# Kernel optimization log

Measured on AMD Instinct MI355X. Metric: run time of the kernel, lower is better.

Reference implementation:

```python
import jax, jax.numpy as jnp
import numpy as np

N_PREV = 250_000   # rows of `features` / `coors` (voxels at previous scale)
N_FULL = 500_000   # full raw points (coors_inv_full / scale_coors_inv length)
V = 65_536         # voxels at current scale
C_IN = 64
C_OUT = 64
SCALE = 2
EPS = 1e-5


def lrelu(x):
    return jnp.where(x > 0, x, 0.1 * x)


def masked_bn(x, mask, gamma, beta):
    # training-mode BatchNorm1d over valid (non-padded) rows only; mask: [M,1]
    n = jnp.maximum(mask.sum(), 1.0)
    mu = (x * mask).sum(0) / n
    var = (((x - mu) * mask) ** 2).sum(0) / n  # biased var, as torch BN
    return gamma * (x - mu) * jax.lax.rsqrt(var + EPS) + beta


def setup_inputs():
    key = jax.random.key(0)
    ks = jax.random.split(key, 16)
    features = jax.random.normal(ks[0], (N_PREV, C_IN), jnp.float32)
    batch = jax.random.randint(ks[1], (N_PREV, 1), 0, 4)
    xy = jax.random.randint(ks[2], (N_PREV, 2), 0, 1000)
    z = jax.random.randint(ks[3], (N_PREV, 1), 0, 60)
    coors = jnp.concatenate([batch, xy, z], axis=1).astype(jnp.int32)
    coors_inv_full = jax.random.randint(ks[4], (N_FULL,), 0, N_PREV, jnp.int32)
    scale_coors_inv = jax.random.randint(ks[5], (N_FULL,), 0, V, jnp.int32)

    def lin(k, i, o):
        return jax.random.normal(k, (i, o), jnp.float32) / np.sqrt(i).astype(np.float32)

    h = C_OUT // 2
    return dict(
        features=features, coors=coors, coors_inv_full=coors_inv_full,
        scale_coors_inv=scale_coors_inv,
        W_in=lin(ks[6], C_IN, C_OUT), b_in=jnp.zeros((C_OUT,), jnp.float32),
        W1=lin(ks[7], C_IN, h), b1=jnp.zeros((h,), jnp.float32),
        g1=jnp.ones((h,), jnp.float32), be1=jnp.zeros((h,), jnp.float32),
        W2=lin(ks[8], h, h), b2=jnp.zeros((h,), jnp.float32),
        g2=jnp.ones((h,), jnp.float32), be2=jnp.zeros((h,), jnp.float32),
        W3=lin(ks[9], h, C_OUT), b3=jnp.zeros((C_OUT,), jnp.float32),
        Wo1=lin(ks[10], 2 * C_OUT, C_OUT), bo1=jnp.zeros((C_OUT,), jnp.float32),
        Wo2=lin(ks[11], C_OUT, C_OUT), bo2=jnp.zeros((C_OUT,), jnp.float32),
    )


def reference(features, coors, coors_inv_full, scale_coors_inv,
              W_in, b_in, W1, b1, g1, be1, W2, b2, g2, be2, W3, b3,
              Wo1, bo1, Wo2, bo2):
    # --- downsample: unique voxel key + scatter_mean (torch.unique return_inverse) ---
    b = coors[:, 0].astype(jnp.int32)
    xyz = coors[:, 1:].astype(jnp.int32) // SCALE
    keys = ((b * 501 + xyz[:, 0]) * 501 + xyz[:, 1]) * 31 + xyz[:, 2]  # < 2^31
    _, inv = jnp.unique(keys, return_inverse=True, size=N_PREV,
                        fill_value=jnp.int32(2**31 - 1))
    cnt = jax.ops.segment_sum(jnp.ones((N_PREV,), jnp.float32), inv,
                              num_segments=N_PREV)
    pooled = jax.ops.segment_sum(features, inv, num_segments=N_PREV) \
        / jnp.maximum(cnt, 1.0)[:, None]
    valid = (cnt > 0).astype(jnp.float32)[:, None]

    # --- identity branch: layer_in ---
    identity = lrelu(features @ W_in + b_in)

    # --- PPmodel on pooled voxels, then gather back by inv ---
    h = masked_bn(lrelu(pooled @ W1 + b1), valid, g1, be1)
    h = masked_bn(lrelu(h @ W2 + b2), valid, g2, be2)
    h = lrelu(h @ W3 + b3)
    out = jnp.concatenate([identity, h[inv]], axis=1)  # [N_PREV, 2*C_OUT]

    # --- gather to full points, layer_out, scatter_mean to scale voxels ---
    gathered = out[coors_inv_full]                      # [N_FULL, 2*C_OUT]
    po = lrelu(gathered @ Wo1 + bo1) @ Wo2 + bo2        # [N_FULL, C_OUT]
    cnt_v = jax.ops.segment_sum(jnp.ones((N_FULL,), jnp.float32),
                                scale_coors_inv, num_segments=V)
    v_feat = jax.ops.segment_sum(po, scale_coors_inv, num_segments=V) \
        / jnp.maximum(cnt_v, 1.0)[:, None]
    return v_feat
```

## Files before the change

### kernel.cpp

```cpp
#include <hip/hip_runtime.h>

#define N_PREV 250000
#define N_FULL 500000
#define NVOX   65536
#define NWORDS (1u<<20)
#define EPSF   1e-5f

typedef __attribute__((ext_vector_type(4)))  short short4v;
typedef __attribute__((ext_vector_type(8)))  short short8v;
typedef __attribute__((ext_vector_type(16))) float f32x16;

__device__ __forceinline__ float lrelu(float x){ return x > 0.0f ? x : 0.1f*x; }
__device__ __forceinline__ short f2bf_rne(float v){
    unsigned u = __float_as_uint(v);
    unsigned r = (u + 0x7fffu + ((u>>16)&1u)) >> 16;
    return (short)r;
}
__device__ __forceinline__ float bf2f(short s){
    return __uint_as_float(((unsigned)(unsigned short)s) << 16);
}

#define OFF_BITMAP   0ul
#define OFF_STATS    4194304ul
#define OFF_CNT      4195328ul
#define OFF_VH       5195328ul
#define OFF_Y        5457472ul
#define ZERO_BYTES   21457472ul
#define OFF_T        5457472ul
#define OFF_P2       37457472ul
#define OFF_PREF     69457472ul
#define OFF_BSUM     73651776ul
#define OFF_BOFF     73655872ul
#define OFF_UCNT     73659968ul
#define OFF_INV      73660224ul
#define OFF_P1       74660224ul
#define OFF_X2       106660224ul
#define WS_NEEDED    138660224ul
#define OFF_CSRJ     0ul
#define OFF_CSRH     2000000ul
#define OFF_VSTART   69457472ul
#define OFF_VNEXT    (OFF_VSTART+262400ul)
#define OFF_VPART    (OFF_VNEXT+262144ul)
#define OFF_VBSUM    (OFF_VPART+262144ul)

__device__ __forceinline__ int voxel_key(int4 c){
    return ((c.x*501 + (c.y>>1))*501 + (c.z>>1))*31 + (c.w>>1);
}

__global__ void k_mark(const int* __restrict__ coors, unsigned* __restrict__ bitmap){
    int i = blockIdx.x*256 + threadIdx.x;
    if(i >= N_PREV) return;
    int4 c = ((const int4*)coors)[i];
    int key = voxel_key(c);
    atomicOr(&bitmap[key>>5], 1u<<(key&31));
}

__global__ void __launch_bounds__(1024) k_scanA(const unsigned* __restrict__ bitmap,
                                                unsigned* __restrict__ pref,
                                                unsigned* __restrict__ bsum){
    __shared__ unsigned sh[1024];
    int tid = threadIdx.x;
    int w = blockIdx.x*1024 + tid;
    unsigned p = __popc(bitmap[w]);
    sh[tid] = p; __syncthreads();
    for(int off=1; off<1024; off<<=1){
        unsigned v = (tid>=off) ? sh[tid-off] : 0u;
        __syncthreads();
        sh[tid] += v;
        __syncthreads();
    }
    pref[w] = sh[tid] - p;
    if(tid==1023) bsum[blockIdx.x] = sh[tid];
}

__global__ void __launch_bounds__(1024) k_scanB(const unsigned* __restrict__ bsum,
                                                unsigned* __restrict__ boff,
                                                unsigned* __restrict__ Ucnt){
    __shared__ unsigned sh[1024];
    int tid = threadIdx.x;
    unsigned p = bsum[tid];
    sh[tid] = p; __syncthreads();
    for(int off=1; off<1024; off<<=1){
        unsigned v = (tid>=off) ? sh[tid-off] : 0u;
        __syncthreads();
        sh[tid] += v;
        __syncthreads();
    }
    boff[tid] = sh[tid] - p;
    if(tid==1023) Ucnt[0] = sh[tid];
}

__global__ void k_vhist(const int* __restrict__ scv, unsigned* __restrict__ vh){
    int p = blockIdx.x*256 + threadIdx.x;
    if(p < N_FULL) atomicAdd(&vh[scv[p]], 1u);
}

__global__ void __launch_bounds__(1024) k_vscanA(const unsigned* __restrict__ vh,
                                                 unsigned* __restrict__ vpart,
                                                 unsigned* __restrict__ vbsum){
    __shared__ unsigned sh[1024];
    int tid = threadIdx.x;
    int w = blockIdx.x*1024 + tid;
    unsigned p = vh[w];
    sh[tid] = p; __syncthreads();
    for(int off=1; off<1024; off<<=1){
        unsigned v = (tid>=off) ? sh[tid-off] : 0u;
        __syncthreads();
        sh[tid] += v;
        __syncthreads();
    }
    vpart[w] = sh[tid] - p;
    if(tid==1023) vbsum[blockIdx.x] = sh[tid];
}

__global__ void k_vscanB(unsigned* __restrict__ vbsum){
    int l = threadIdx.x;
    unsigned v = vbsum[l], orig = v;
    for(int off=1; off<64; off<<=1){
        unsigned o = __shfl_up(v, off);
        if(l>=off) v += o;
    }
    vbsum[l] = v - orig;
}

__global__ void __launch_bounds__(1024) k_vfix(const unsigned* __restrict__ vpart,
                                               const unsigned* __restrict__ vbsum,
                                               unsigned* __restrict__ vstart,
                                               unsigned* __restrict__ vnext){
    int w = blockIdx.x*1024 + threadIdx.x;
    unsigned s = vpart[w] + vbsum[w>>10];
    vstart[w] = s; vnext[w] = s;
    if(w == NVOX-1) vstart[NVOX] = N_FULL;
}

__global__ void k_fill(const int* __restrict__ cif, const int* __restrict__ scv,
                       const int* __restrict__ inv, unsigned* __restrict__ vnext,
                       int* __restrict__ csr_j, int* __restrict__ csr_h){
    int p = blockIdx.x*256 + threadIdx.x;
    if(p >= N_FULL) return;
    int jp = cif[p];
    unsigned pos = atomicAdd(&vnext[scv[p]], 1u);
    csr_j[pos] = jp;
    csr_h[pos] = inv[jp];
}

__global__ void __launch_bounds__(256) k_p1f(const float* __restrict__ feat,
        const int* __restrict__ coors, const unsigned* __restrict__ bitmap,
        const unsigned* __restrict__ pref, const unsigned* __restrict__ boff,
        const float* __restrict__ Win, const float* __restrict__ bin,
        const float* __restrict__ Wo1, const float* __restrict__ W1,
        unsigned short* __restrict__ P1, int* __restrict__ inv,
        float* __restrict__ cnt, unsigned short* __restrict__ yb){
    __shared__ __align__(16) short Ah[64*68];
    __shared__ __align__(16) short Al[64*68];
    __shared__ float ysh[64][33];
    __shared__ int rksh[64];
    int tid = threadIdx.x;
    int wave = tid >> 6, l = tid & 63;
    int g = l >> 5, c = l & 31;
    int rowhalf = (wave >> 1) * 32, colhalf = (wave & 1) * 32;

    {
        int col = tid >> 2, kseg = (tid & 3) * 16;
        short hi[16], lo[16];
        #pragma unroll
        for(int j=0;j<16;++j){
            float v = Win[(kseg+j)*64 + col];
            short h = f2bf_rne(v);
            hi[j] = h; lo[j] = f2bf_rne(v - bf2f(h));
        }
        #pragma unroll
        for(int i=0;i<4;++i){
            *(short4v*)&Ah[col*68 + kseg + 4*i] = *(short4v*)&hi[4*i];
            *(short4v*)&Al[col*68 + kseg + 4*i] = *(short4v*)&lo[4*i];
        }
    }
    __syncthreads();
    short8v w1h[4], w1l[4];
    #pragma unroll
    for(int s=0;s<4;++s){
        int base = (colhalf + c)*68 + s*16 + g*4;
        ((short4v*)&w1h[s])[0] = *(short4v*)&Ah[base];
        ((short4v*)&w1h[s])[1] = *(short4v*)&Ah[base + 8];
        ((short4v*)&w1l[s])[0] = *(short4v*)&Al[base];
        ((short4v*)&w1l[s])[1] = *(short4v*)&Al[base + 8];
    }
    __syncthreads();
    {
        int col = tid >> 2, kseg = (tid & 3) * 16;
        short hi[16];
        #pragma unroll
        for(int j=0;j<16;++j) hi[j] = f2bf_rne(Wo1[(kseg+j)*64 + col]);
        #pragma unroll
        for(int i=0;i<4;++i)
            *(short4v*)&Ah[col*68 + kseg + 4*i] = *(short4v*)&hi[4*i];
    }
    __syncthreads();
    short8v w2h[4];
    #pragma unroll
    for(int s=0;s<4;++s){
        int base = (colhalf + c)*68 + s*16 + g*4;
        ((short4v*)&w2h[s])[0] = *(short4v*)&Ah[base];
        ((short4v*)&w2h[s])[1] = *(short4v*)&Ah[base + 8];
    }
    __syncthreads();
    if(tid < 128){
        int col = tid >> 2, kseg = (tid & 3) * 16;
        short hi[16], lo[16];
        #pragma unroll
        for(int j=0;j<16;++j){
            float v = W1[(kseg+j)*32 + col];
            short h = f2bf_rne(v);
            hi[j] = h; lo[j] = f2bf_rne(v - bf2f(h));
        }
        #pragma unroll
        for(int i=0;i<4;++i){
            *(short4v*)&Ah[col*68 + kseg + 4*i] = *(short4v*)&hi[4*i];
            *(short4v*)&Al[col*68 + kseg + 4*i] = *(short4v*)&lo[4*i];
        }
    }
    __syncthreads();
    short8v w0h[4], w0l[4];
    #pragma unroll
    for(int s=0;s<4;++s){
        int base = c*68 + s*16 + g*4;
        ((short4v*)&w0h[s])[0] = *(short4v*)&Ah[base];
        ((short4v*)&w0h[s])[1] = *(short4v*)&Ah[base + 8];
        ((short4v*)&w0l[s])[0] = *(short4v*)&Al[base];
        ((short4v*)&w0l[s])[1] = *(short4v*)&Al[base + 8];
    }
    __syncthreads();

    float bc1 = bin[colhalf + c];

    const int NT = (N_PREV + 63) / 64;
    for(int tile = blockIdx.x; tile < NT; tile += gridDim.x){
        int rbase = tile * 64;
        {
            int row = tid >> 2, kseg = (tid & 3) * 16;
            int grow = rbase + row;
            float fv[16];
            if(grow < N_PREV){
                const float4* fp = (const float4*)&feat[grow*64 + kseg];
                *(float4*)&fv[0]  = fp[0];
                *(float4*)&fv[4]  = fp[1];
                *(float4*)&fv[8]  = fp[2];
                *(float4*)&fv[12] = fp[3];
            } else {
                #pragma unroll
                for(int j=0;j<16;++j) fv[j]=0.f;
            }
            short hi[16], lo[16];
            #pragma unroll
            for(int j=0;j<16;++j){
                short h = f2bf_rne(fv[j]);
                hi[j] = h; lo[j] = f2bf_rne(fv[j] - bf2f(h));
            }
            #pragma unroll
            for(int i=0;i<4;++i){
                *(short4v*)&Ah[row*68 + kseg + 4*i] = *(short4v*)&hi[4*i];
                *(short4v*)&Al[row*68 + kseg + 4*i] = *(short4v*)&lo[4*i];
            }
        }
        if(tid < 64){
            int grow = rbase + tid;
            if(grow < N_PREV){
                int4 c4 = ((const int4*)coors)[grow];
                int key = voxel_key(c4);
                int w = key>>5, b = key&31;
                int rank = (int)(boff[w>>10] + pref[w]) + __popc(bitmap[w] & ((1u<<b)-1u));
                rksh[tid] = rank;
                inv[grow] = rank;
                atomicAdd(&cnt[rank], 1.0f);
            } else rksh[tid] = -1;
        }
        __syncthreads();
        f32x16 acc;
        #pragma unroll
        for(int i=0;i<16;++i) acc[i]=0.f;
        #pragma unroll
        for(int s=0;s<4;++s){
            int abase = (rowhalf + c)*68 + s*16 + g*4;
            short8v ah, al;
            ((short4v*)&ah)[0] = *(short4v*)&Ah[abase];
            ((short4v*)&ah)[1] = *(short4v*)&Ah[abase + 8];
            ((short4v*)&al)[0] = *(short4v*)&Al[abase];
            ((short4v*)&al)[1] = *(short4v*)&Al[abase + 8];
            acc = __builtin_amdgcn_mfma_f32_32x32x16_bf16(ah, w1h[s], acc, 0,0,0);
            acc = __builtin_amdgcn_mfma_f32_32x32x16_bf16(al, w1h[s], acc, 0,0,0);
            acc = __builtin_amdgcn_mfma_f32_32x32x16_bf16(ah, w1l[s], acc, 0,0,0);
        }
        f32x16 accY;
        #pragma unroll
        for(int i=0;i<16;++i) accY[i]=0.f;
        if(wave < 2){
            #pragma unroll
            for(int s=0;s<4;++s){
                int abase = (wave*32 + c)*68 + s*16 + g*4;
                short8v ah, al;
                ((short4v*)&ah)[0] = *(short4v*)&Ah[abase];
                ((short4v*)&ah)[1] = *(short4v*)&Ah[abase + 8];
                ((short4v*)&al)[0] = *(short4v*)&Al[abase];
                ((short4v*)&al)[1] = *(short4v*)&Al[abase + 8];
                accY = __builtin_amdgcn_mfma_f32_32x32x16_bf16(ah, w0h[s], accY, 0,0,0);
                accY = __builtin_amdgcn_mfma_f32_32x32x16_bf16(al, w0h[s], accY, 0,0,0);
                accY = __builtin_amdgcn_mfma_f32_32x32x16_bf16(ah, w0l[s], accY, 0,0,0);
            }
        }
        __syncthreads();
        #pragma unroll
        for(int r=0;r<16;++r){
            int row = rowhalf + (r&3) + 8*(r>>2) + 4*g;
            float v = acc[r] + bc1;
            v = v > 0.f ? v : 0.1f*v;
            Ah[row*68 + colhalf + c] = f2bf_rne(v);
        }
        if(wave < 2){
            #pragma unroll
            for(int r=0;r<16;++r){
                int row = wave*32 + (r&3) + 8*(r>>2) + 4*g;
                ysh[row][c] = accY[r];
            }
        }
        __syncthreads();
        f32x16 acc2;
        #pragma unroll
        for(int i=0;i<16;++i) acc2[i]=0.f;
        #pragma unroll
        for(int s=0;s<4;++s){
            int abase = (rowhalf + c)*68 + s*16 + g*4;
            short8v ah;
            ((short4v*)&ah)[0] = *(short4v*)&Ah[abase];
            ((short4v*)&ah)[1] = *(short4v*)&Ah[abase + 8];
            acc2 = __builtin_amdgcn_mfma_f32_32x32x16_bf16(ah, w2h[s], acc2, 0,0,0);
        }
        #pragma unroll
        for(int r=0;r<16;++r){
            int grow = rbase + rowhalf + (r&3) + 8*(r>>2) + 4*g;
            if(grow < N_PREV) P1[grow*64 + colhalf + c] = (unsigned short)f2bf_rne(acc2[r]);
        }
        #pragma unroll
        for(int q=0;q<4;++q){
            int e = q*256 + tid;
            int row = e >> 4, pr = e & 15;
            int rk = rksh[row];
            if(rk >= 0){
                unsigned h0 = (unsigned)(unsigned short)f2bf_rne(ysh[row][2*pr]);
                unsigned h1 = (unsigned)(unsigned short)f2bf_rne(ysh[row][2*pr+1]);
                unsigned pk = h0 | (h1 << 16);
                unsigned short* addr = yb + (size_t)rk*32 + 2*pr;
                asm volatile("global_atomic_pk_add_bf16 %0, %1, off"
                             :: "v"(addr), "v"(pk) : "memory");
            }
        }
        __syncthreads();
    }
}

__global__ void __launch_bounds__(256) k_bn1(const unsigned short* __restrict__ yb,
        const float* __restrict__ cnt, const unsigned* __restrict__ Ucnt,
        const float* __restrict__ b1, float* __restrict__ stats){
    __shared__ float sst[32], qst[32];
    int tid = threadIdx.x;
    if(tid < 32){ sst[tid]=0.f; qst[tid]=0.f; }
    __syncthreads();
    int U = (int)Ucnt[0];
    int total = U*4;
    int c8 = (tid&3)*8;
    float bb[8];
    #pragma unroll
    for(int j=0;j<8;++j) bb[j] = b1[c8+j];
    float s[8], q[8];
    #pragma unroll
    for(int j=0;j<8;++j){ s[j]=0.f; q[j]=0.f; }
    for(int e = blockIdx.x*256 + tid; e < total; e += gridDim.x*256){
        int row = e >> 2;
        float rv = 1.0f/cnt[row];
        uint4 a = ((const uint4*)yb)[e];
        unsigned wv[4] = {a.x,a.y,a.z,a.w};
        #pragma unroll
        for(int k=0;k<4;++k){
            float lo = __uint_as_float(wv[k]<<16);
            float hi = __uint_as_float(wv[k]&0xffff0000u);
            float v0 = lrelu(lo*rv + bb[2*k]);
            float v1 = lrelu(hi*rv + bb[2*k+1]);
            s[2*k]+=v0; q[2*k]+=v0*v0;
            s[2*k+1]+=v1; q[2*k+1]+=v1*v1;
        }
    }
    #pragma unroll
    for(int j=0;j<8;++j){ atomicAdd(&sst[c8+j], s[j]); atomicAdd(&qst[c8+j], q[j]); }
    __syncthreads();
    if(tid < 32){ atomicAdd(&stats[tid], sst[tid]); atomicAdd(&stats[32+tid], qst[tid]); }
}

__global__ void k_bnfin(const unsigned* __restrict__ Ucnt, const float* __restrict__ g,
                        float* __restrict__ stats, int off){
    int c = threadIdx.x;
    if(c>=32) return;
    float n = (float)max(Ucnt[0], 1u);
    float mu = stats[off+c]/n;
    float var = stats[off+32+c]/n - mu*mu;
    stats[off+64+c] = mu;
    stats[off+96+c] = g[c]*rsqrtf(var + EPSF);
}

__global__ void __launch_bounds__(256) k_ppm2(const unsigned short* __restrict__ yb,
        const float* __restrict__ cnt, const unsigned* __restrict__ Ucnt,
        const float* __restrict__ W2, const float* __restrict__ b1i,
        const float* __restrict__ b2, const float* __restrict__ be1,
        unsigned short* __restrict__ x2b, float* __restrict__ stats){
    __shared__ __align__(16) short Ah[128*36];
    __shared__ __align__(16) short Al[128*36];
    __shared__ float ash[32], bbsh[32], b1sh[32];
    __shared__ float red[4][64];
    int tid = threadIdx.x;
    int wave = tid >> 6, l = tid & 63;
    int g = l >> 5, c = l & 31;

    if(tid < 32){
        float mu=stats[64+tid], sc=stats[96+tid];
        ash[tid]=sc; bbsh[tid]=be1[tid]-mu*sc;
        b1sh[tid]=b1i[tid];
    }
    if(tid >= 64 && tid < 128){
        int t = tid - 64;
        int col = t >> 1, kseg = (t & 1) * 16;
        short hi[16], lo[16];
        #pragma unroll
        for(int j=0;j<16;++j){
            float v = W2[(kseg+j)*32 + col];
            short h = f2bf_rne(v);
            hi[j] = h; lo[j] = f2bf_rne(v - bf2f(h));
        }
        #pragma unroll
        for(int i=0;i<4;++i){
            *(short4v*)&Ah[col*36 + kseg + 4*i] = *(short4v*)&hi[4*i];
            *(short4v*)&Al[col*36 + kseg + 4*i] = *(short4v*)&lo[4*i];
        }
    }
    __syncthreads();
    short8v wh[2], wl[2];
    #pragma unroll
    for(int s=0;s<2;++s){
        int base = c*36 + s*16 + g*4;
        ((short4v*)&wh[s])[0] = *(short4v*)&Ah[base];
        ((short4v*)&wh[s])[1] = *(short4v*)&Ah[base + 8];
        ((short4v*)&wl[s])[0] = *(short4v*)&Al[base];
        ((short4v*)&wl[s])[1] = *(short4v*)&Al[base + 8];
    }
    __syncthreads();

    int U = (int)Ucnt[0];
    float bc = b2[c];
    float s_acc = 0.f, q_acc = 0.f;

    const int NT = (N_PREV + 127) / 128;
    for(int tile = blockIdx.x; tile < NT; tile += gridDim.x){
        int rbase = tile * 128;
        if(rbase >= U) break;
        {
            int row = tid >> 1, kseg = (tid & 1) * 16;
            int grow = rbase + row;
            float fv[16];
            if(grow < U){
                float rv = 1.0f/cnt[grow];
                uint4 a0 = *(const uint4*)&yb[grow*32 + kseg];
                uint4 a1 = *(const uint4*)&yb[grow*32 + kseg + 8];
                unsigned wv[8] = {a0.x,a0.y,a0.z,a0.w,a1.x,a1.y,a1.z,a1.w};
                #pragma unroll
                for(int k=0;k<8;++k){
                    float lo = __uint_as_float(wv[k]<<16);
                    float hi = __uint_as_float(wv[k]&0xffff0000u);
                    float v0 = lrelu(lo*rv + b1sh[kseg+2*k]);
                    float v1 = lrelu(hi*rv + b1sh[kseg+2*k+1]);
                    fv[2*k]   = v0*ash[kseg+2*k]   + bbsh[kseg+2*k];
                    fv[2*k+1] = v1*ash[kseg+2*k+1] + bbsh[kseg+2*k+1];
                }
            } else {
                #pragma unroll
                for(int j=0;j<16;++j) fv[j]=0.f;
            }
            short hi[16], lo[16];
            #pragma unroll
            for(int j=0;j<16;++j){
                short h = f2bf_rne(fv[j]);
                hi[j] = h; lo[j] = f2bf_rne(fv[j] - bf2f(h));
            }
            #pragma unroll
            for(int i=0;i<4;++i){
                *(short4v*)&Ah[row*36 + kseg + 4*i] = *(short4v*)&hi[4*i];
                *(short4v*)&Al[row*36 + kseg + 4*i] = *(short4v*)&lo[4*i];
            }
        }
        __syncthreads();
        f32x16 acc;
        #pragma unroll
        for(int i=0;i<16;++i) acc[i]=0.f;
        #pragma unroll
        for(int s=0;s<2;++s){
            int abase = (wave*32 + c)*36 + s*16 + g*4;
            short8v ah, al;
            ((short4v*)&ah)[0] = *(short4v*)&Ah[abase];
            ((short4v*)&ah)[1] = *(short4v*)&Ah[abase + 8];
            ((short4v*)&al)[0] = *(short4v*)&Al[abase];
            ((short4v*)&al)[1] = *(short4v*)&Al[abase + 8];
            acc = __builtin_amdgcn_mfma_f32_32x32x16_bf16(ah, wh[s], acc, 0,0,0);
            acc = __builtin_amdgcn_mfma_f32_32x32x16_bf16(al, wh[s], acc, 0,0,0);
            acc = __builtin_amdgcn_mfma_f32_32x32x16_bf16(ah, wl[s], acc, 0,0,0);
        }
        #pragma unroll
        for(int r=0;r<16;++r){
            int rl = wave*32 + (r&3) + 8*(r>>2) + 4*g;
            int grow = rbase + rl;
            if(grow < U){
                float v = acc[r] + bc;
                v = v > 0.f ? v : 0.1f*v;
                x2b[grow*32 + c] = (unsigned short)f2bf_rne(v);
                s_acc += v; q_acc += v*v;
            }
        }
        __syncthreads();
    }
    s_acc += __shfl_xor(s_acc, 32);
    q_acc += __shfl_xor(q_acc, 32);
    if(l < 32){ red[wave][c] = s_acc; red[wave][32+c] = q_acc; }
    __syncthreads();
    if(tid < 64){
        float t = red[0][tid]+red[1][tid]+red[2][tid]+red[3][tid];
        atomicAdd(&stats[128+tid], t);
    }
}

__global__ void __launch_bounds__(256) k_ppm3(const unsigned short* __restrict__ x2b,
        const unsigned* __restrict__ Ucnt, const float* __restrict__ W3,
        const float* __restrict__ b3, const float* __restrict__ be2,
        const float* __restrict__ Wo1, unsigned short* __restrict__ P2,
        const float* __restrict__ stats){
    __shared__ __align__(16) short Ah[64*36];
    __shared__ __align__(16) short Al[64*36];
    __shared__ __align__(16) short Ih[64*68];
    __shared__ __align__(16) short Il[64*36];
    __shared__ float ash[32], bbsh[32];
    int tid = threadIdx.x;
    int wave = tid >> 6, l = tid & 63;
    int g = l >> 5, c = l & 31;
    int rowhalf = (wave >> 1) * 32, colhalf = (wave & 1) * 32;

    if(tid < 32){
        float mu=stats[192+tid], sc=stats[224+tid];
        ash[tid]=sc; bbsh[tid]=be2[tid]-mu*sc;
    }
    if(tid >= 128){
        int t = tid - 128;
        int col = t >> 1, kseg = (t & 1) * 16;
        short hi[16], lo[16];
        #pragma unroll
        for(int j=0;j<16;++j){
            float v = W3[(kseg+j)*64 + col];
            short h = f2bf_rne(v);
            hi[j] = h; lo[j] = f2bf_rne(v - bf2f(h));
        }
        #pragma unroll
        for(int i=0;i<4;++i){
            *(short4v*)&Ih[col*36 + kseg + 4*i] = *(short4v*)&hi[4*i];
            *(short4v*)&Il[col*36 + kseg + 4*i] = *(short4v*)&lo[4*i];
        }
    }
    __syncthreads();
    short8v w3h[2], w3l[2];
    #pragma unroll
    for(int s=0;s<2;++s){
        int base = (colhalf + c)*36 + s*16 + g*4;
        ((short4v*)&w3h[s])[0] = *(short4v*)&Ih[base];
        ((short4v*)&w3h[s])[1] = *(short4v*)&Ih[base + 8];
        ((short4v*)&w3l[s])[0] = *(short4v*)&Il[base];
        ((short4v*)&w3l[s])[1] = *(short4v*)&Il[base + 8];
    }
    __syncthreads();
    {
        int col = tid >> 2, kseg = (tid & 3) * 16;
        short hi[16];
        #pragma unroll
        for(int j=0;j<16;++j) hi[j] = f2bf_rne(Wo1[4096 + (kseg+j)*64 + col]);
        #pragma unroll
        for(int i=0;i<4;++i)
            *(short4v*)&Ih[col*68 + kseg + 4*i] = *(short4v*)&hi[4*i];
    }
    __syncthreads();
    short8v w2h[4];
    #pragma unroll
    for(int s=0;s<4;++s){
        int base = (colhalf + c)*68 + s*16 + g*4;
        ((short4v*)&w2h[s])[0] = *(short4v*)&Ih[base];
        ((short4v*)&w2h[s])[1] = *(short4v*)&Ih[base + 8];
    }
    __syncthreads();

    int U = (int)Ucnt[0];
    float bc3 = b3[colhalf + c];

    const int NT = (N_PREV + 63) / 64;
    for(int tile = blockIdx.x; tile < NT; tile += gridDim.x){
        int rbase = tile * 64;
        if(rbase >= U) break;
        if(tid < 128){
            int row = tid >> 1, kseg = (tid & 1) * 16;
            int grow = rbase + row;
            float fv[16];
            if(grow < U){
                uint4 a0 = *(const uint4*)&x2b[grow*32 + kseg];
                uint4 a1 = *(const uint4*)&x2b[grow*32 + kseg + 8];
                unsigned wv[8] = {a0.x,a0.y,a0.z,a0.w,a1.x,a1.y,a1.z,a1.w};
                #pragma unroll
                for(int k=0;k<8;++k){
                    float lo = __uint_as_float(wv[k]<<16);
                    float hi = __uint_as_float(wv[k]&0xffff0000u);
                    fv[2*k]   = lo*ash[kseg+2*k]   + bbsh[kseg+2*k];
                    fv[2*k+1] = hi*ash[kseg+2*k+1] + bbsh[kseg+2*k+1];
                }
            } else {
                #pragma unroll
                for(int j=0;j<16;++j) fv[j]=0.f;
            }
            short hi[16], lo[16];
            #pragma unroll
            for(int j=0;j<16;++j){
                short h = f2bf_rne(fv[j]);
                hi[j] = h; lo[j] = f2bf_rne(fv[j] - bf2f(h));
            }
            #pragma unroll
            for(int i=0;i<4;++i){
                *(short4v*)&Ah[row*36 + kseg + 4*i] = *(short4v*)&hi[4*i];
                *(short4v*)&Al[row*36 + kseg + 4*i] = *(short4v*)&lo[4*i];
            }
        }
        __syncthreads();
        f32x16 acc;
        #pragma unroll
        for(int i=0;i<16;++i) acc[i]=0.f;
        #pragma unroll
        for(int s=0;s<2;++s){
            int abase = (rowhalf + c)*36 + s*16 + g*4;
            short8v ah, al;
            ((short4v*)&ah)[0] = *(short4v*)&Ah[abase];
            ((short4v*)&ah)[1] = *(short4v*)&Ah[abase + 8];
            ((short4v*)&al)[0] = *(short4v*)&Al[abase];
            ((short4v*)&al)[1] = *(short4v*)&Al[abase + 8];
            acc = __builtin_amdgcn_mfma_f32_32x32x16_bf16(ah, w3h[s], acc, 0,0,0);
            acc = __builtin_amdgcn_mfma_f32_32x32x16_bf16(al, w3h[s], acc, 0,0,0);
            acc = __builtin_amdgcn_mfma_f32_32x32x16_bf16(ah, w3l[s], acc, 0,0,0);
        }
        #pragma unroll
        for(int r=0;r<16;++r){
            int row = rowhalf + (r&3) + 8*(r>>2) + 4*g;
            float v = acc[r] + bc3;
            v = v > 0.f ? v : 0.1f*v;
            Ih[row*68 + colhalf + c] = f2bf_rne(v);
        }
        __syncthreads();
        f32x16 acc2;
        #pragma unroll
        for(int i=0;i<16;++i) acc2[i]=0.f;
        #pragma unroll
        for(int s=0;s<4;++s){
            int abase = (rowhalf + c)*68 + s*16 + g*4;
            short8v ah;
            ((short4v*)&ah)[0] = *(short4v*)&Ih[abase];
            ((short4v*)&ah)[1] = *(short4v*)&Ih[abase + 8];
            acc2 = __builtin_amdgcn_mfma_f32_32x32x16_bf16(ah, w2h[s], acc2, 0,0,0);
        }
        #pragma unroll
        for(int r=0;r<16;++r){
            int grow = rbase + rowhalf + (r&3) + 8*(r>>2) + 4*g;
            if(grow < U) P2[grow*64 + colhalf + c] = (unsigned short)f2bf_rne(acc2[r]);
        }
        __syncthreads();
    }
}

__global__ void __launch_bounds__(256) k_vox(const unsigned* __restrict__ vstart,
        const int* __restrict__ csr_j, const int* __restrict__ csr_h,
        const unsigned short* __restrict__ P1, const unsigned short* __restrict__ P2,
        const float* __restrict__ bo1, float* __restrict__ T){
    int tid = threadIdx.x;
    int wib = tid>>6, lane = tid&63;
    float b1c = bo1[lane];
    int wglobal = blockIdx.x*4 + wib;
    for(int vq=0; vq<4; ++vq){
        int vox = wglobal*4 + vq;
        int s = (int)vstart[vox], e = (int)vstart[vox+1];
        float acc = 0.f;
        for(int i=s; i<e; i+=64){
            int n = min(e-i, 64);
            int jv=0, hv=0;
            if(lane<n){ jv = csr_j[i+lane]; hv = csr_h[i+lane]; }
            for(int q0=0; q0<n; q0+=8){
                float pa[8], pb[8];
                #pragma unroll
                for(int t=0;t<8;++t){
                    int qq = q0 + t;
                    qq = (qq < n) ? qq : q0;
                    int j = __shfl(jv, qq);
                    int h = __shfl(hv, qq);
                    pa[t] = bf2f((short)P1[(size_t)j*64 + lane]);
                    pb[t] = bf2f((short)P2[(size_t)h*64 + lane]);
                }
                #pragma unroll
                for(int t=0;t<8;++t){
                    if(q0 + t < n){
                        float g = pa[t] + pb[t] + b1c;
                        acc += (g>0.f) ? g : 0.1f*g;
                    }
                }
            }
        }
        T[(size_t)vox*64 + lane] = acc;
    }
}

__global__ void __launch_bounds__(256) k_wo2(const float* __restrict__ T,
        const unsigned* __restrict__ vstart, const float* __restrict__ Wo2,
        const float* __restrict__ bo2, float* __restrict__ out){
    __shared__ __align__(16) short Ah[64*68];
    __shared__ __align__(16) short Al[64*68];
    __shared__ float csh[64];
    int tid = threadIdx.x;
    int wave = tid >> 6, l = tid & 63;
    int g = l >> 5, c = l & 31;
    int rowhalf = (wave >> 1) * 32, colhalf = (wave & 1) * 32;

    {
        int col = tid >> 2, kseg = (tid & 3) * 16;
        short hi[16], lo[16];
        #pragma unroll
        for(int j=0;j<16;++j){
            float v = Wo2[(kseg+j)*64 + col];
            short h = f2bf_rne(v);
            hi[j] = h; lo[j] = f2bf_rne(v - bf2f(h));
        }
        #pragma unroll
        for(int i=0;i<4;++i){
            *(short4v*)&Ah[col*68 + kseg + 4*i] = *(short4v*)&hi[4*i];
            *(short4v*)&Al[col*68 + kseg + 4*i] = *(short4v*)&lo[4*i];
        }
    }
    __syncthreads();
    short8v wh[4], wl[4];
    #pragma unroll
    for(int s=0;s<4;++s){
        int base = (colhalf + c)*68 + s*16 + g*4;
        ((short4v*)&wh[s])[0] = *(short4v*)&Ah[base];
        ((short4v*)&wh[s])[1] = *(short4v*)&Ah[base + 8];
        ((short4v*)&wl[s])[0] = *(short4v*)&Al[base];
        ((short4v*)&wl[s])[1] = *(short4v*)&Al[base + 8];
    }
    __syncthreads();

    float bo2c = bo2[colhalf + c];

    const int NT = NVOX / 64;
    for(int tile = blockIdx.x; tile < NT; tile += gridDim.x){
        int rbase = tile * 64;
        {
            int row = tid >> 2, kseg = (tid & 3) * 16;
            const float4* fp = (const float4*)&T[(size_t)(rbase + row)*64 + kseg];
            float fv[16];
            *(float4*)&fv[0]  = fp[0];
            *(float4*)&fv[4]  = fp[1];
            *(float4*)&fv[8]  = fp[2];
            *(float4*)&fv[12] = fp[3];
            short hi[16], lo[16];
            #pragma unroll
            for(int j=0;j<16;++j){
                short h = f2bf_rne(fv[j]);
                hi[j] = h; lo[j] = f2bf_rne(fv[j] - bf2f(h));
            }
            #pragma unroll
            for(int i=0;i<4;++i){
                *(short4v*)&Ah[row*68 + kseg + 4*i] = *(short4v*)&hi[4*i];
                *(short4v*)&Al[row*68 + kseg + 4*i] = *(short4v*)&lo[4*i];
            }
        }
        if(tid < 64){
            int vox = rbase + tid;
            csh[tid] = (float)(vstart[vox+1] - vstart[vox]);
        }
        __syncthreads();
        f32x16 acc;
        #pragma unroll
        for(int i=0;i<16;++i) acc[i]=0.f;
        #pragma unroll
        for(int s=0;s<4;++s){
            int abase = (rowhalf + c)*68 + s*16 + g*4;
            short8v ah, al;
            ((short4v*)&ah)[0] = *(short4v*)&Ah[abase];
            ((short4v*)&ah)[1] = *(short4v*)&Ah[abase + 8];
            ((short4v*)&al)[0] = *(short4v*)&Al[abase];
            ((short4v*)&al)[1] = *(short4v*)&Al[abase + 8];
            acc = __builtin_amdgcn_mfma_f32_32x32x16_bf16(ah, wh[s], acc, 0,0,0);
            acc = __builtin_amdgcn_mfma_f32_32x32x16_bf16(al, wh[s], acc, 0,0,0);
            acc = __builtin_amdgcn_mfma_f32_32x32x16_bf16(ah, wl[s], acc, 0,0,0);
        }
        #pragma unroll
        for(int r=0;r<16;++r){
            int row = rowhalf + (r&3) + 8*(r>>2) + 4*g;
            float cv = csh[row];
            float rv = (cv > 0.f) ? 1.0f/cv : 0.f;
            float bz = (cv > 0.f) ? bo2c : 0.f;
            out[(size_t)(rbase + row)*64 + colhalf + c] = acc[r]*rv + bz;
        }
        __syncthreads();
    }
}

extern "C" void kernel_launch(void* const* d_in, const int* in_sizes, int n_in,
                              void* d_out, int out_size, void* d_ws, size_t ws_size,
                              hipStream_t stream) {
    if(ws_size < WS_NEEDED) return;

    const float* features = (const float*)d_in[0];
    const int*   coors    = (const int*)d_in[1];
    const int*   cif      = (const int*)d_in[2];
    const int*   scv      = (const int*)d_in[3];
    const float* W_in     = (const float*)d_in[4];
    const float* b_in     = (const float*)d_in[5];
    const float* W1       = (const float*)d_in[6];
    const float* b1       = (const float*)d_in[7];
    const float* g1       = (const float*)d_in[8];
    const float* be1      = (const float*)d_in[9];
    const float* W2       = (const float*)d_in[10];
    const float* b2       = (const float*)d_in[11];
    const float* g2       = (const float*)d_in[12];
    const float* be2      = (const float*)d_in[13];
    const float* W3       = (const float*)d_in[14];
    const float* b3       = (const float*)d_in[15];
    const float* Wo1      = (const float*)d_in[16];
    const float* bo1      = (const float*)d_in[17];
    const float* Wo2      = (const float*)d_in[18];
    const float* bo2      = (const float*)d_in[19];

    char* ws = (char*)d_ws;
    unsigned* bitmap = (unsigned*)(ws + OFF_BITMAP);
    float*    stats  = (float*)(ws + OFF_STATS);
    float*    cnt    = (float*)(ws + OFF_CNT);
    unsigned* vh     = (unsigned*)(ws + OFF_VH);
    unsigned short* yb = (unsigned short*)(ws + OFF_Y);
    float*    T      = (float*)(ws + OFF_T);
    unsigned short* P2 = (unsigned short*)(ws + OFF_P2);
    unsigned* pref   = (unsigned*)(ws + OFF_PREF);
    unsigned* bsum   = (unsigned*)(ws + OFF_BSUM);
    unsigned* boff   = (unsigned*)(ws + OFF_BOFF);
    unsigned* Ucnt   = (unsigned*)(ws + OFF_UCNT);
    int*      inv    = (int*)(ws + OFF_INV);
    unsigned short* P1 = (unsigned short*)(ws + OFF_P1);
    unsigned short* x2b = (unsigned short*)(ws + OFF_X2);
    int*      csr_j  = (int*)(ws + OFF_CSRJ);
    int*      csr_h  = (int*)(ws + OFF_CSRH);
    unsigned* vstart = (unsigned*)(ws + OFF_VSTART);
    unsigned* vnext  = (unsigned*)(ws + OFF_VNEXT);
    unsigned* vpart  = (unsigned*)(ws + OFF_VPART);
    unsigned* vbsum  = (unsigned*)(ws + OFF_VBSUM);

    hipMemsetAsync(d_ws, 0, ZERO_BYTES, stream);

    k_mark  <<<(N_PREV+255)/256, 256, 0, stream>>>(coors, bitmap);
    k_scanA <<<1024, 1024, 0, stream>>>(bitmap, pref, bsum);
    k_scanB <<<1, 1024, 0, stream>>>(bsum, boff, Ucnt);
    k_p1f   <<<1024, 256, 0, stream>>>(features, coors, bitmap, pref, boff,
                                       W_in, b_in, Wo1, W1, P1, inv, cnt, yb);
    k_vhist <<<(N_FULL+255)/256, 256, 0, stream>>>(scv, vh);
    k_vscanA<<<64, 1024, 0, stream>>>(vh, vpart, vbsum);
    k_vscanB<<<1, 64, 0, stream>>>(vbsum);
    k_vfix  <<<64, 1024, 0, stream>>>(vpart, vbsum, vstart, vnext);
    k_fill  <<<(N_FULL+255)/256, 256, 0, stream>>>(cif, scv, inv, vnext, csr_j, csr_h);
    k_bn1   <<<1024, 256, 0, stream>>>(yb, cnt, Ucnt, b1, stats);
    k_bnfin <<<1, 32, 0, stream>>>(Ucnt, g1, stats, 0);
    k_ppm2  <<<1024, 256, 0, stream>>>(yb, cnt, Ucnt, W2, b1, b2, be1, x2b, stats);
    k_bnfin <<<1, 32, 0, stream>>>(Ucnt, g2, stats, 128);
    k_ppm3  <<<1024, 256, 0, stream>>>(x2b, Ucnt, W3, b3, be2, Wo1, P2, stats);
    k_vox   <<<NVOX/16, 256, 0, stream>>>(vstart, csr_j, csr_h, P1, P2, bo1, T);
    k_wo2   <<<256, 256, 0, stream>>>(T, vstart, Wo2, bo2, (float*)d_out);
}
```

Measured before the change: 276.2 us.

## Merge small kernels and prefetch next voxel's CSR indices in k_vox

Folds the voxel histogram into the bitmap-marking kernel, moves the 64-entry block-sum scan into k_vfix, and computes the BatchNorm finalisation inside k_ppm2/k_ppm3 instead of separate one-block kernels. This removes four kernel launches and their serialization gaps. k_vox now loads the CSR indices of the next voxel while processing the current one, hiding index-load latency. Every block of k_ppm2/k_ppm3 recomputes the small BN finalisation redundantly, which adds a little work per block.

```diff
diff --git a/kernel.cpp b/kernel.cpp
--- a/kernel.cpp
+++ b/kernel.cpp
@@ -47,12 +47,15 @@
     return ((c.x*501 + (c.y>>1))*501 + (c.z>>1))*31 + (c.w>>1);
 }
 
-__global__ void k_mark(const int* __restrict__ coors, unsigned* __restrict__ bitmap){
+__global__ void k_mark(const int* __restrict__ coors, const int* __restrict__ scv,
+                       unsigned* __restrict__ bitmap, unsigned* __restrict__ vh){
     int i = blockIdx.x*256 + threadIdx.x;
-    if(i >= N_PREV) return;
-    int4 c = ((const int4*)coors)[i];
-    int key = voxel_key(c);
-    atomicOr(&bitmap[key>>5], 1u<<(key&31));
+    if(i < N_PREV){
+        int4 c = ((const int4*)coors)[i];
+        int key = voxel_key(c);
+        atomicOr(&bitmap[key>>5], 1u<<(key&31));
+    }
+    if(i < N_FULL) atomicAdd(&vh[scv[i]], 1u);
 }
 
 __global__ void __launch_bounds__(1024) k_scanA(const unsigned* __restrict__ bitmap,
@@ -90,11 +93,6 @@
     if(tid==1023) Ucnt[0] = sh[tid];
 }
 
-__global__ void k_vhist(const int* __restrict__ scv, unsigned* __restrict__ vh){
-    int p = blockIdx.x*256 + threadIdx.x;
-    if(p < N_FULL) atomicAdd(&vh[scv[p]], 1u);
-}
-
 __global__ void __launch_bounds__(1024) k_vscanA(const unsigned* __restrict__ vh,
                                                  unsigned* __restrict__ vpart,
                                                  unsigned* __restrict__ vbsum){
@@ -113,22 +111,23 @@
     if(tid==1023) vbsum[blockIdx.x] = sh[tid];
 }
 
-__global__ void k_vscanB(unsigned* __restrict__ vbsum){
-    int l = threadIdx.x;
-    unsigned v = vbsum[l], orig = v;
-    for(int off=1; off<64; off<<=1){
-        unsigned o = __shfl_up(v, off);
-        if(l>=off) v += o;
-    }
-    vbsum[l] = v - orig;
-}
-
 __global__ void __launch_bounds__(1024) k_vfix(const unsigned* __restrict__ vpart,
                                                const unsigned* __restrict__ vbsum,
                                                unsigned* __restrict__ vstart,
                                                unsigned* __restrict__ vnext){
-    int w = blockIdx.x*1024 + threadIdx.x;
-    unsigned s = vpart[w] + vbsum[w>>10];
+    __shared__ unsigned bo[64];
+    int tid = threadIdx.x;
+    if(tid < 64){
+        unsigned v = vbsum[tid], orig = v;
+        for(int off=1; off<64; off<<=1){
+            unsigned o = __shfl_up(v, off);
+            if(tid>=off) v += o;
+        }
+        bo[tid] = v - orig;
+    }
+    __syncthreads();
+    int w = blockIdx.x*1024 + tid;
+    unsigned s = vpart[w] + bo[w>>10];
     vstart[w] = s; vnext[w] = s;
     if(w == NVOX-1) vstart[NVOX] = N_FULL;
 }
@@ -394,22 +393,12 @@
     if(tid < 32){ atomicAdd(&stats[tid], sst[tid]); atomicAdd(&stats[32+tid], qst[tid]); }
 }
 
-__global__ void k_bnfin(const unsigned* __restrict__ Ucnt, const float* __restrict__ g,
-                        float* __restrict__ stats, int off){
-    int c = threadIdx.x;
-    if(c>=32) return;
-    float n = (float)max(Ucnt[0], 1u);
-    float mu = stats[off+c]/n;
-    float var = stats[off+32+c]/n - mu*mu;
-    stats[off+64+c] = mu;
-    stats[off+96+c] = g[c]*rsqrtf(var + EPSF);
-}
-
 __global__ void __launch_bounds__(256) k_ppm2(const unsigned short* __restrict__ yb,
         const float* __restrict__ cnt, const unsigned* __restrict__ Ucnt,
         const float* __restrict__ W2, const float* __restrict__ b1i,
         const float* __restrict__ b2, const float* __restrict__ be1,
-        unsigned short* __restrict__ x2b, float* __restrict__ stats){
+        const float* __restrict__ g1, unsigned short* __restrict__ x2b,
+        float* __restrict__ stats){
     __shared__ __align__(16) short Ah[128*36];
     __shared__ __align__(16) short Al[128*36];
     __shared__ float ash[32], bbsh[32], b1sh[32];
@@ -419,7 +408,10 @@
     int g = l >> 5, c = l & 31;
 
     if(tid < 32){
-        float mu=stats[64+tid], sc=stats[96+tid];
+        float n = (float)max(Ucnt[0], 1u);
+        float mu = stats[tid]/n;
+        float var = stats[32+tid]/n - mu*mu;
+        float sc = g1[tid]*rsqrtf(var + EPSF);
         ash[tid]=sc; bbsh[tid]=be1[tid]-mu*sc;
         b1sh[tid]=b1i[tid];
     }
@@ -535,8 +527,8 @@
 __global__ void __launch_bounds__(256) k_ppm3(const unsigned short* __restrict__ x2b,
         const unsigned* __restrict__ Ucnt, const float* __restrict__ W3,
         const float* __restrict__ b3, const float* __restrict__ be2,
-        const float* __restrict__ Wo1, unsigned short* __restrict__ P2,
-        const float* __restrict__ stats){
+        const float* __restrict__ g2, const float* __restrict__ Wo1,
+        unsigned short* __restrict__ P2, const float* __restrict__ stats){
     __shared__ __align__(16) short Ah[64*36];
     __shared__ __align__(16) short Al[64*36];
     __shared__ __align__(16) short Ih[64*68];
@@ -548,7 +540,10 @@
     int rowhalf = (wave >> 1) * 32, colhalf = (wave & 1) * 32;
 
     if(tid < 32){
-        float mu=stats[192+tid], sc=stats[224+tid];
+        float n = (float)max(Ucnt[0], 1u);
+        float mu = stats[128+tid]/n;
+        float var = stats[160+tid]/n - mu*mu;
+        float sc = g2[tid]*rsqrtf(var + EPSF);
         ash[tid]=sc; bbsh[tid]=be2[tid]-mu*sc;
     }
     if(tid >= 128){
@@ -686,23 +681,40 @@
     int tid = threadIdx.x;
     int wib = tid>>6, lane = tid&63;
     float b1c = bo1[lane];
-    int wglobal = blockIdx.x*4 + wib;
+    int vox0 = (blockIdx.x*4 + wib)*4;
+    int s = (int)vstart[vox0];
+    int e = (int)vstart[vox0+1];
+    int jv = 0, hv = 0;
+    {
+        int n0 = min(e - s, 64);
+        if(lane < n0){ jv = csr_j[s+lane]; hv = csr_h[s+lane]; }
+    }
     for(int vq=0; vq<4; ++vq){
-        int vox = wglobal*4 + vq;
-        int s = (int)vstart[vox], e = (int)vstart[vox+1];
+        int vox = vox0 + vq;
+        int cs = s, ce = e, cjv = jv, chv = hv;
+        if(vq < 3){
+            s = e;
+            e = (int)vstart[vox+2];
+            int n2 = min(e - s, 64);
+            jv = 0; hv = 0;
+            if(lane < n2){ jv = csr_j[s+lane]; hv = csr_h[s+lane]; }
+        }
         float acc = 0.f;
-        for(int i=s; i<e; i+=64){
-            int n = min(e-i, 64);
-            int jv=0, hv=0;
-            if(lane<n){ jv = csr_j[i+lane]; hv = csr_h[i+lane]; }
+        for(int i=cs; i<ce; i+=64){
+            int n = min(ce-i, 64);
+            int jj = cjv, hh = chv;
+            if(i > cs){
+                jj = 0; hh = 0;
+                if(lane < n){ jj = csr_j[i+lane]; hh = csr_h[i+lane]; }
+            }
             for(int q0=0; q0<n; q0+=8){
                 float pa[8], pb[8];
                 #pragma unroll
                 for(int t=0;t<8;++t){
                     int qq = q0 + t;
                     qq = (qq < n) ? qq : q0;
-                    int j = __shfl(jv, qq);
-                    int h = __shfl(hv, qq);
+                    int j = __shfl(jj, qq);
+                    int h = __shfl(hh, qq);
                     pa[t] = bf2f((short)P1[(size_t)j*64 + lane]);
                     pb[t] = bf2f((short)P2[(size_t)h*64 + lane]);
                 }
@@ -864,21 +876,17 @@
 
     hipMemsetAsync(d_ws, 0, ZERO_BYTES, stream);
 
-    k_mark  <<<(N_PREV+255)/256, 256, 0, stream>>>(coors, bitmap);
+    k_mark  <<<(N_FULL+255)/256, 256, 0, stream>>>(coors, scv, bitmap, vh);
     k_scanA <<<1024, 1024, 0, stream>>>(bitmap, pref, bsum);
     k_scanB <<<1, 1024, 0, stream>>>(bsum, boff, Ucnt);
     k_p1f   <<<1024, 256, 0, stream>>>(features, coors, bitmap, pref, boff,
                                        W_in, b_in, Wo1, W1, P1, inv, cnt, yb);
-    k_vhist <<<(N_FULL+255)/256, 256, 0, stream>>>(scv, vh);
     k_vscanA<<<64, 1024, 0, stream>>>(vh, vpart, vbsum);
-    k_vscanB<<<1, 64, 0, stream>>>(vbsum);
     k_vfix  <<<64, 1024, 0, stream>>>(vpart, vbsum, vstart, vnext);
     k_fill  <<<(N_FULL+255)/256, 256, 0, stream>>>(cif, scv, inv, vnext, csr_j, csr_h);
     k_bn1   <<<1024, 256, 0, stream>>>(yb, cnt, Ucnt, b1, stats);
-    k_bnfin <<<1, 32, 0, stream>>>(Ucnt, g1, stats, 0);
-    k_ppm2  <<<1024, 256, 0, stream>>>(yb, cnt, Ucnt, W2, b1, b2, be1, x2b, stats);
-    k_bnfin <<<1, 32, 0, stream>>>(Ucnt, g2, stats, 128);
-    k_ppm3  <<<1024, 256, 0, stream>>>(x2b, Ucnt, W3, b3, be2, Wo1, P2, stats);
+    k_ppm2  <<<1024, 256, 0, stream>>>(yb, cnt, Ucnt, W2, b1, b2, be1, g1, x2b, stats);
+    k_ppm3  <<<1024, 256, 0, stream>>>(x2b, Ucnt, W3, b3, be2, g2, Wo1, P2, stats);
     k_vox   <<<NVOX/16, 256, 0, stream>>>(vstart, csr_j, csr_h, P1, P2, bo1, T);
     k_wo2   <<<256, 256, 0, stream>>>(T, vstart, Wo2, bo2, (float*)d_out);
 }
```

Measured after the change: 269.1 us (median of 2 runs). 2.6% less time.
